# Kernel tuning notes

Measured on AMD Instinct MI355X. Metric: run time of the kernel, lower is better.

The kernel has to match this reference:

```python
import jax, jax.numpy as jnp
import numpy as np

IN_DIM = 16
OUT_DIM = 16
BASIS_DIM = 4
N, M = 4, 96


def setup_inputs() -> dict:
    key = jax.random.key(0)
    k1, k2 = jax.random.split(key)
    x = jax.random.normal(k1, (N, IN_DIM, M), dtype=jnp.float32)
    std = np.sqrt(2.0 / (IN_DIM + OUT_DIM + BASIS_DIM)).astype(np.float32)
    coefs = std * jax.random.normal(k2, (IN_DIM, OUT_DIM, BASIS_DIM), dtype=jnp.float32)
    bias = jnp.zeros((1, OUT_DIM, 1, 1, 1), dtype=jnp.float32)
    return {"x": x, "coefs": coefs, "bias": bias}


def reference(x, coefs, bias):
    # Eq1to3: out[n,s,i,j,k] = sum_d c[d,s,0] x[n,d,i] + c[d,s,1] x[n,d,j]
    #                         + c[d,s,2] x[n,d,k] + c[d,s,3] sum_t x[n,d,t]  + bias
    # Equivalent to einsum('dsb,ndbijk->nsijk', coefs, eset_ops_1_to_3(x)) but
    # without materializing the (n,d,4,m,m,m) basis tensor.
    Y = jnp.einsum('ndi,dsb->nsbi', x, coefs[:, :, :3])        # (n, out, 3, m)
    S = jnp.einsum('nd,ds->ns', x.sum(axis=-1), coefs[:, :, 3])  # (n, out)
    out = (Y[:, :, 0, :, None, None]   # x_i broadcast over j,k
           + Y[:, :, 1, None, :, None]  # x_j broadcast over i,k
           + Y[:, :, 2, None, None, :]  # x_k broadcast over i,j
           + S[:, :, None, None, None]  # set-sum broadcast
           + bias)
    return out  # (n, out_dim, m, m, m)
```

## Files before the change

### kernel.cpp

```cpp
#include <hip/hip_runtime.h>

#define M_DIM   96
#define IN_DIM  16
#define OUT_DIM 16
#define N_BATCH 4
#define PLANE4  (M_DIM * M_DIM / 4)

typedef float f4 __attribute__((ext_vector_type(4)));

__global__ __launch_bounds__(256) void eq13_kernel(
    const float* __restrict__ x,
    const float* __restrict__ coefs,
    const float* __restrict__ bias,
    f4* __restrict__ out4)
{
    __shared__ float s_y0[M_DIM];
    __shared__ float s_y1[M_DIM];
    __shared__ __align__(16) float s_y2[M_DIM];
    __shared__ float s_red[M_DIM];
    __shared__ float s_S;

    const int bid = blockIdx.x;
    const int ns  = bid / M_DIM;
    const int i   = bid - ns * M_DIM;
    const int n   = ns >> 4;
    const int s   = ns & 15;
    const int t   = threadIdx.x;

    if (t < M_DIM) {
        float y0 = 0.f, y1 = 0.f, y2 = 0.f, y3 = 0.f;
        const float* xb = x + (size_t)n * IN_DIM * M_DIM + t;
        const float* cb = coefs + s * 4;
        #pragma unroll
        for (int d = 0; d < IN_DIM; ++d) {
            float xv = xb[d * M_DIM];
            f4 c4 = *(const f4*)(cb + d * OUT_DIM * 4);
            y0 = fmaf(xv, c4.x, y0);
            y1 = fmaf(xv, c4.y, y1);
            y2 = fmaf(xv, c4.z, y2);
            y3 = fmaf(xv, c4.w, y3);
        }
        s_y0[t]  = y0;
        s_y1[t]  = y1;
        s_y2[t]  = y2;
        s_red[t] = y3;
    }
    __syncthreads();

    if (t < 64) {
        float v = s_red[t] + ((t < 32) ? s_red[t + 64] : 0.f);
        #pragma unroll
        for (int off = 32; off; off >>= 1) v += __shfl_down(v, off);
        if (t == 0) s_S = v + bias[s];
    }
    __syncthreads();

    const float  base = s_y0[i] + s_S;
    const f4*    y2v  = (const f4*)s_y2;
    f4* dst = out4 + (size_t)bid * PLANE4;

    #pragma unroll
    for (int it = 0; it < 9; ++it) {
        int   c  = t + it * 256;
        int   j  = c / 24;
        int   kq = c - j * 24;
        float v  = base + s_y1[j];
        f4    f  = y2v[kq];
        f.x += v; f.y += v; f.z += v; f.w += v;
        dst[c] = f;
    }
}

extern "C" void kernel_launch(void* const* d_in, const int* in_sizes, int n_in,
                              void* d_out, int out_size, void* d_ws, size_t ws_size,
                              hipStream_t stream) {
    const float* x     = (const float*)d_in[0];
    const float* coefs = (const float*)d_in[1];
    const float* bias  = (const float*)d_in[2];
    f4* out4 = (f4*)d_out;

    const int grid = N_BATCH * OUT_DIM * M_DIM;
    eq13_kernel<<<grid, 256, 0, stream>>>(x, coefs, bias, out4);
}
```

Before: 219.5 us.

## Process three i-planes per block and compute set-sum in every wave

Each block now writes three consecutive i-planes instead of one, cutting the grid by a factor of three. The per-block projection of x onto coefs and the (j,k) partial sums are computed once and reused across all three planes. The set-sum reduction now runs redundantly in every wavefront with xor-shuffles, which removes the second barrier. The cost is more registers per thread for the cached tile and fewer blocks available to hide store latency.

```diff
diff --git a/kernel.cpp b/kernel.cpp
--- a/kernel.cpp
+++ b/kernel.cpp
@@ -5,6 +5,7 @@
 #define OUT_DIM 16
 #define N_BATCH 4
 #define PLANE4  (M_DIM * M_DIM / 4)
+#define PPB     3
 
 typedef float f4 __attribute__((ext_vector_type(4)));
 
@@ -18,14 +19,15 @@
     __shared__ float s_y1[M_DIM];
     __shared__ __align__(16) float s_y2[M_DIM];
     __shared__ float s_red[M_DIM];
-    __shared__ float s_S;
 
     const int bid = blockIdx.x;
-    const int ns  = bid / M_DIM;
-    const int i   = bid - ns * M_DIM;
+    const int ns  = bid >> 5;
+    const int ig  = (bid & 31) * PPB;
     const int n   = ns >> 4;
     const int s   = ns & 15;
     const int t   = threadIdx.x;
+
+    const float bs = bias[s];
 
     if (t < M_DIM) {
         float y0 = 0.f, y1 = 0.f, y2 = 0.f, y3 = 0.f;
@@ -47,27 +49,38 @@
     }
     __syncthreads();
 
-    if (t < 64) {
-        float v = s_red[t] + ((t < 32) ? s_red[t + 64] : 0.f);
+    {
+        const int lane = t & 63;
+        float v = s_red[lane] + ((lane < 32) ? s_red[lane + 64] : 0.f);
         #pragma unroll
-        for (int off = 32; off; off >>= 1) v += __shfl_down(v, off);
-        if (t == 0) s_S = v + bias[s];
-    }
-    __syncthreads();
+        for (int off = 32; off; off >>= 1) v += __shfl_xor(v, off);
+        s_red[0] = s_red[0];
+        const float S = v + bs;
 
-    const float  base = s_y0[i] + s_S;
-    const f4*    y2v  = (const f4*)s_y2;
-    f4* dst = out4 + (size_t)bid * PLANE4;
+        const f4* y2v = (const f4*)s_y2;
+        f4 g[9];
+        #pragma unroll
+        for (int it = 0; it < 9; ++it) {
+            int   c  = t + it * 256;
+            int   j  = c / 24;
+            int   kq = c - j * 24;
+            float w  = s_y1[j];
+            f4    f  = y2v[kq];
+            f.x += w; f.y += w; f.z += w; f.w += w;
+            g[it] = f;
+        }
 
-    #pragma unroll
-    for (int it = 0; it < 9; ++it) {
-        int   c  = t + it * 256;
-        int   j  = c / 24;
-        int   kq = c - j * 24;
-        float v  = base + s_y1[j];
-        f4    f  = y2v[kq];
-        f.x += v; f.y += v; f.z += v; f.w += v;
-        dst[c] = f;
+        f4* dst = out4 + (size_t)(ns * M_DIM + ig) * PLANE4;
+        #pragma unroll
+        for (int p = 0; p < PPB; ++p) {
+            const float base = s_y0[ig + p] + S;
+            #pragma unroll
+            for (int it = 0; it < 9; ++it) {
+                f4 f = g[it];
+                f.x += base; f.y += base; f.z += base; f.w += base;
+                dst[p * PLANE4 + t + it * 256] = f;
+            }
+        }
     }
 }
 
@@ -79,6 +92,6 @@
     const float* bias  = (const float*)d_in[2];
     f4* out4 = (f4*)d_out;
 
-    const int grid = N_BATCH * OUT_DIM * M_DIM;
+    const int grid = N_BATCH * OUT_DIM * (M_DIM / PPB);
     eq13_kernel<<<grid, 256, 0, stream>>>(x, coefs, bias, out4);
 }
```

New measurement: 221.5 us. No clear change (+0.9%).
